# Performance work log

Measured on AMD Instinct MI355X. Metric: run time of the kernel, lower is better.

## Reference

```python
import jax, jax.numpy as jnp
import numpy as np

B, N, BS, H, DH, L, FF, V, R = 1, 4096, 64, 12, 64, 4, 3072, 30522, 3
D = H * DH
M = N // BS
NEG = -10000.0


def layernorm(x, g, b, eps=1e-5):
    mu = x.mean(-1, keepdims=True)
    var = ((x - mu) ** 2).mean(-1, keepdims=True)
    return (x - mu) * jax.lax.rsqrt(var + eps) * g + b


def bigbird_attention(q, k, v, band_mask, from_mask, to_mask, blocked_mask, rand_attn):
    # q,k,v: [b,h,n,d]; band_mask [b,1,m-4,BS,3BS]; to_mask [b,1,1,n]; from_mask [b,1,n,1]
    b, h, n, d = q.shape
    m = n // BS
    r = rand_attn.shape[-1]
    sc = 1.0 / jnp.sqrt(jnp.float32(d))
    qb = q.reshape(b, h, m, BS, d)
    kb = k.reshape(b, h, m, BS, d)
    vb = v.reshape(b, h, m, BS, d)
    hid = jnp.arange(h)[:, None, None]
    gk = kb[:, hid, rand_attn].reshape(b, h, m - 2, r * BS, d)  # gathered random keys
    gv = vb[:, hid, rand_attn].reshape(b, h, m - 2, r * BS, d)
    rand_to = blocked_mask[:, rand_attn].reshape(b, h, m - 2, r * BS)
    rand_mask = jnp.einsum('blq,bhlk->bhlqk', blocked_mask[:, 1:-1], rand_to)  # [b,h,m-2,BS,rBS]

    # first block: dense over all keys (global)
    s = jnp.einsum('bhqd,bhkd->bhqk', qb[:, :, 0], k) * sc + (1.0 - to_mask) * NEG
    c_first = jnp.einsum('bhqk,bhkd->bhqd', jax.nn.softmax(s, axis=-1), v)

    # second block: blocks 0,1,2, last, + random row 0
    k2 = jnp.concatenate([kb[:, :, 0], kb[:, :, 1], kb[:, :, 2], kb[:, :, -1], gk[:, :, 0]], axis=2)
    v2 = jnp.concatenate([vb[:, :, 0], vb[:, :, 1], vb[:, :, 2], vb[:, :, -1], gv[:, :, 0]], axis=2)
    s = jnp.einsum('bhqd,bhkd->bhqk', qb[:, :, 1], k2) * sc
    seq_pad = jnp.concatenate([to_mask[..., :3 * BS], to_mask[..., -BS:],
                               jnp.ones((b, 1, 1, r * BS), s.dtype)], axis=3)
    rnd_pad = jnp.concatenate([jnp.ones((b, h, BS, 4 * BS), s.dtype), rand_mask[:, :, 0]], axis=3)
    s = s + (1.0 - jnp.minimum(seq_pad, rnd_pad)) * NEG
    c_second = jnp.einsum('bhqk,bhkd->bhqd', jax.nn.softmax(s, axis=-1), v2)

    # middle blocks: first-global + 3-block band + random + last-global
    mq = qb[:, :, 2:-2]  # [b,h,m-4,BS,d]
    exp_k = jnp.concatenate([kb[:, :, 1:-3], kb[:, :, 2:-2], kb[:, :, 3:-1]], axis=3)
    exp_v = jnp.concatenate([vb[:, :, 1:-3], vb[:, :, 2:-2], vb[:, :, 3:-1]], axis=3)
    inner = jnp.einsum('bhlqd,bhlkd->bhlqk', mq, exp_k) * sc + (1.0 - band_mask) * NEG
    randp = jnp.einsum('bhlqd,bhlkd->bhlqk', mq, gk[:, :, 1:-1]) * sc + (1.0 - rand_mask[:, :, 1:-1]) * NEG
    firstp = jnp.einsum('bhlqd,bhkd->bhlqk', mq, kb[:, :, 0]) * sc + (1.0 - to_mask[:, :, None, :, :BS]) * NEG
    lastp = jnp.einsum('bhlqd,bhkd->bhlqk', mq, kb[:, :, -1]) * sc + (1.0 - to_mask[:, :, None, :, -BS:]) * NEG
    w = jax.nn.softmax(jnp.concatenate([firstp, inner, randp, lastp], axis=-1), axis=-1)
    c_mid = jnp.einsum('bhlqk,bhlkd->bhlqd', w[..., BS:4 * BS], exp_v)
    c_mid = c_mid + jnp.einsum('bhlqk,bhlkd->bhlqd', w[..., 4 * BS:4 * BS + r * BS], gv[:, :, 1:-1])
    c_mid = c_mid + jnp.einsum('bhlqk,bhkd->bhlqd', w[..., :BS], vb[:, :, 0])
    c_mid = c_mid + jnp.einsum('bhlqk,bhkd->bhlqd', w[..., -BS:], vb[:, :, -1])

    # second-to-last block: block 0, last 3 blocks, + random row -1
    k3 = jnp.concatenate([kb[:, :, 0], kb[:, :, -3], kb[:, :, -2], kb[:, :, -1], gk[:, :, -1]], axis=2)
    v3 = jnp.concatenate([vb[:, :, 0], vb[:, :, -3], vb[:, :, -2], vb[:, :, -1], gv[:, :, -1]], axis=2)
    s = jnp.einsum('bhqd,bhkd->bhqk', qb[:, :, -2], k3) * sc
    seq_pad = jnp.concatenate([to_mask[..., :BS], to_mask[..., -3 * BS:],
                               jnp.ones((b, 1, 1, r * BS), s.dtype)], axis=3)
    rnd_pad = jnp.concatenate([jnp.ones((b, h, BS, 4 * BS), s.dtype), rand_mask[:, :, -1]], axis=3)
    s = s + (1.0 - jnp.minimum(seq_pad, rnd_pad)) * NEG
    c_sl = jnp.einsum('bhqk,bhkd->bhqd', jax.nn.softmax(s, axis=-1), v3)

    # last block: dense over all keys (global)
    s = jnp.einsum('bhqd,bhkd->bhqk', qb[:, :, -1], k) * sc + (1.0 - to_mask) * NEG
    c_last = jnp.einsum('bhqk,bhkd->bhqd', jax.nn.softmax(s, axis=-1), v)

    ctx = jnp.concatenate([c_first[:, :, None], c_second[:, :, None], c_mid,
                           c_sl[:, :, None], c_last[:, :, None]], axis=2)
    ctx = ctx.reshape(b, h, n, d) * from_mask
    return ctx.transpose(0, 2, 1, 3).reshape(b, n, h * d)


def forward(input_ids, mask, rand_attn, emb_word, emb_pos, emb_ln_g, emb_ln_b,
            Wq, bq, Wk, bk, Wv, bv, Wo, bo, ln1_g, ln1_b, W1, b1, W2, b2, ln2_g, ln2_b):
    b, n = input_ids.shape
    m = n // BS
    x = emb_word[input_ids] + emb_pos[None, :n]
    x = layernorm(x, emb_ln_g, emb_ln_b)
    blocked_mask = mask.reshape(b, m, BS)
    exp_to = jnp.concatenate([blocked_mask[:, 1:-3], blocked_mask[:, 2:-2], blocked_mask[:, 3:-1]], axis=2)
    band_mask = jnp.einsum('blq,blk->blqk', blocked_mask[:, 2:-2], exp_to)[:, None]
    from_mask = mask.reshape(b, 1, n, 1)
    to_mask = mask.reshape(b, 1, 1, n)
    for i in range(L):
        q = (x @ Wq[i] + bq[i]).reshape(b, n, H, DH).transpose(0, 2, 1, 3)
        k = (x @ Wk[i] + bk[i]).reshape(b, n, H, DH).transpose(0, 2, 1, 3)
        v = (x @ Wv[i] + bv[i]).reshape(b, n, H, DH).transpose(0, 2, 1, 3)
        a = bigbird_attention(q, k, v, band_mask, from_mask, to_mask, blocked_mask, rand_attn)
        a = a @ Wo[i] + bo[i]
        x = layernorm(x + a, ln1_g[i], ln1_b[i])  # dropout is identity in eval
        f = jax.nn.gelu(x @ W1[i] + b1[i], approximate=False) @ W2[i] + b2[i]
        x = layernorm(x + f, ln2_g[i], ln2_b[i])
    return x


def setup_inputs() -> dict:
    key = jax.random.key(0)
    ks = jax.random.split(key, 12)
    s = 0.02
    nrm = lambda k, shape: jax.random.normal(k, shape, jnp.float32) * s
    rng = np.random.default_rng(0)
    rand_attn = jnp.asarray(rng.integers(1, M - 1, size=(H, M - 2, R)), jnp.int32)
    return {
        'input_ids': jax.random.randint(ks[0], (B, N), 0, V),
        'mask': jnp.ones((B, N), jnp.float32),
        'rand_attn': rand_attn,
        'emb_word': nrm(ks[1], (V, D)),
        'emb_pos': nrm(ks[2], (N, D)),
        'emb_ln_g': jnp.ones((D,), jnp.float32), 'emb_ln_b': jnp.zeros((D,), jnp.float32),
        'Wq': nrm(ks[3], (L, D, D)), 'bq': jnp.zeros((L, D), jnp.float32),
        'Wk': nrm(ks[4], (L, D, D)), 'bk': jnp.zeros((L, D), jnp.float32),
        'Wv': nrm(ks[5], (L, D, D)), 'bv': jnp.zeros((L, D), jnp.float32),
        'Wo': nrm(ks[6], (L, D, D)), 'bo': jnp.zeros((L, D), jnp.float32),
        'ln1_g': jnp.ones((L, D), jnp.float32), 'ln1_b': jnp.zeros((L, D), jnp.float32),
        'W1': nrm(ks[7], (L, D, FF)), 'b1': jnp.zeros((L, FF), jnp.float32),
        'W2': nrm(ks[8], (L, FF, D)), 'b2': jnp.zeros((L, D), jnp.float32),
        'ln2_g': jnp.ones((L, D), jnp.float32), 'ln2_b': jnp.zeros((L, D), jnp.float32),
    }


def reference(input_ids, mask, rand_attn, emb_word, emb_pos, emb_ln_g, emb_ln_b,
              Wq, bq, Wk, bk, Wv, bv, Wo, bo, ln1_g, ln1_b, W1, b1, W2, b2, ln2_g, ln2_b):
    return forward(input_ids, mask, rand_attn, emb_word, emb_pos, emb_ln_g, emb_ln_b,
                   Wq, bq, Wk, bk, Wv, bv, Wo, bo, ln1_g, ln1_b, W1, b1, W2, b2, ln2_g, ln2_b)
```

## Files before the change

### kernel.cpp

```cpp
#include <hip/hip_runtime.h>
#include <hip/hip_bf16.h>
#include <math.h>

#define NTOK   4096
#define DMODEL 768
#define NHEAD  12
#define DHEAD  64
#define NLAYER 4
#define DFF    3072
#define NBLK   64
#define NEGC   -10000.0f

using frag8 = __attribute__((ext_vector_type(8))) short;
using f32x4 = __attribute__((ext_vector_type(4))) float;

typedef __attribute__((address_space(3))) void       lds_void;
typedef const __attribute__((address_space(1))) void gbl_void;

__device__ __forceinline__ void gload_lds16(const void* g, void* l) {
  __builtin_amdgcn_global_load_lds((gbl_void*)g, (lds_void*)l, 16, 0, 0);
}

__device__ __forceinline__ float block_sum256(float v) {
  __shared__ float tmp[4];
  #pragma unroll
  for (int o = 32; o > 0; o >>= 1) v += __shfl_down(v, o, 64);
  __syncthreads();
  if ((threadIdx.x & 63) == 0) tmp[threadIdx.x >> 6] = v;
  __syncthreads();
  return tmp[0] + tmp[1] + tmp[2] + tmp[3];
}

__global__ __launch_bounds__(256) void embed_ln_kernel(
    const int* __restrict__ ids, const float* __restrict__ emb_word,
    const float* __restrict__ emb_pos, const float* __restrict__ g,
    const float* __restrict__ b, float* __restrict__ x,
    __hip_bfloat16* __restrict__ xb)
{
  const int n = blockIdx.x;
  const int tid = threadIdx.x;
  const int id = ids[n];
  float v[3];
  #pragma unroll
  for (int j = 0; j < 3; ++j) {
    int d = tid + j * 256;
    v[j] = emb_word[(size_t)id * DMODEL + d] + emb_pos[(size_t)n * DMODEL + d];
  }
  float mu = block_sum256(v[0] + v[1] + v[2]) * (1.0f / DMODEL);
  float var = 0.f;
  #pragma unroll
  for (int j = 0; j < 3; ++j) { float t = v[j] - mu; var += t * t; }
  var = block_sum256(var) * (1.0f / DMODEL);
  float rs = rsqrtf(var + 1e-5f);
  #pragma unroll
  for (int j = 0; j < 3; ++j) {
    int d = tid + j * 256;
    float o = (v[j] - mu) * rs * g[d] + b[d];
    x[(size_t)n * DMODEL + d] = o;
    xb[(size_t)n * DMODEL + d] = (__hip_bfloat16)o;
  }
}

__global__ __launch_bounds__(256) void add_ln_red_kernel(
    const float* __restrict__ xin, const float* __restrict__ P, size_t ps,
    int nparts, const float* __restrict__ bias2,
    const float* __restrict__ g, const float* __restrict__ b,
    float* __restrict__ dst, __hip_bfloat16* __restrict__ dstb)
{
  const int n = blockIdx.x;
  const int tid = threadIdx.x;
  float v[3];
  #pragma unroll
  for (int j = 0; j < 3; ++j) {
    int d = tid + j * 256;
    float s = xin[(size_t)n * DMODEL + d] + bias2[d];
    for (int z = 0; z < nparts; ++z)
      s += P[(size_t)z * ps + (size_t)n * DMODEL + d];
    v[j] = s;
  }
  float mu = block_sum256(v[0] + v[1] + v[2]) * (1.0f / DMODEL);
  float var = 0.f;
  #pragma unroll
  for (int j = 0; j < 3; ++j) { float t = v[j] - mu; var += t * t; }
  var = block_sum256(var) * (1.0f / DMODEL);
  float rs = rsqrtf(var + 1e-5f);
  #pragma unroll
  for (int j = 0; j < 3; ++j) {
    int d = tid + j * 256;
    float ov = (v[j] - mu) * rs * g[d] + b[d];
    dst[(size_t)n * DMODEL + d] = ov;
    dstb[(size_t)n * DMODEL + d] = (__hip_bfloat16)ov;
  }
}

__global__ __launch_bounds__(256) void transpose_w_kernel(
    const float* __restrict__ W, __hip_bfloat16* __restrict__ WT, int K, int N)
{
  __shared__ float tile[32][33];
  const int n0 = blockIdx.x * 32;
  const int k0 = blockIdx.y * 32;
  const int c = threadIdx.x & 31;
  const int r0 = threadIdx.x >> 5;
  #pragma unroll
  for (int i = 0; i < 4; ++i) {
    int r = r0 + i * 8;
    tile[r][c] = W[(size_t)(k0 + r) * N + n0 + c];
  }
  __syncthreads();
  #pragma unroll
  for (int i = 0; i < 4; ++i) {
    int r = r0 + i * 8;
    WT[(size_t)(n0 + r) * K + k0 + c] = (__hip_bfloat16)tile[c][r];
  }
}

__global__ __launch_bounds__(256) void pack_bias_kernel(
    const float* __restrict__ bq, const float* __restrict__ bk,
    const float* __restrict__ bv, float* __restrict__ dst)
{
  int t = blockIdx.x * 256 + threadIdx.x;
  if (t < 3 * DMODEL)
    dst[t] = (t < DMODEL) ? bq[t] : (t < 2 * DMODEL ? bk[t - DMODEL] : bv[t - 2 * DMODEL]);
}

__global__ __launch_bounds__(256) void gemm_bf16_kernel(
    const __hip_bfloat16* __restrict__ A, int lda,
    const __hip_bfloat16* __restrict__ BT, int ldb,
    const float* __restrict__ bias,
    float* __restrict__ Cf, size_t cfStride,
    __hip_bfloat16* __restrict__ Cb,
    int Kpart, int ldC, int do_gelu)
{
  __shared__ __hip_bfloat16 Als[2][64 * 32];
  __shared__ __hip_bfloat16 Bls[2][128 * 32];
  const int tid = threadIdx.x;

  const int gx = gridDim.x;
  const int nwg = gx * gridDim.y;
  const int orig = blockIdx.y * gx + blockIdx.x;
  const int q = nwg >> 3, r = nwg & 7;
  const int xcd = orig & 7, loc = orig >> 3;
  const int wg = (xcd < r ? xcd * (q + 1) : r * (q + 1) + (xcd - r) * q) + loc;
  const int bm = (wg % gx) * 64;
  const int bn = (wg / gx) * 128;
  const int z  = blockIdx.z;
  const int koff = z * Kpart;

  const int wave = tid >> 6, lane = tid & 63;
  const int wm = (wave >> 1) * 32, wn = (wave & 1) * 64;
  const int lm = lane & 15, quad = lane >> 4;

  const int rA = wave * 16 + (lane >> 2);
  const int kc = (lane & 3) * 8;

  const __hip_bfloat16* Ar  = A  + (size_t)(bm + rA) * lda + koff + kc;
  const __hip_bfloat16* Br0 = BT + (size_t)(bn + rA) * ldb + koff + kc;
  const __hip_bfloat16* Br1 = BT + (size_t)(bn + 64 + rA) * ldb + koff + kc;

  f32x4 acc[2][4];
  #pragma unroll
  for (int i = 0; i < 2; ++i)
    #pragma unroll
    for (int j = 0; j < 4; ++j)
      acc[i][j] = (f32x4){0.f, 0.f, 0.f, 0.f};

  gload_lds16(Ar,  &Als[0][rA * 32 + kc]);
  gload_lds16(Br0, &Bls[0][rA * 32 + kc]);
  gload_lds16(Br1, &Bls[0][(64 + rA) * 32 + kc]);

  int p = 0;
  for (int k0 = 0; k0 < Kpart; k0 += 32, p ^= 1) {
    __syncthreads();
    const int kn = k0 + 32;
    if (kn < Kpart) {
      gload_lds16(Ar + kn,  &Als[p ^ 1][rA * 32 + kc]);
      gload_lds16(Br0 + kn, &Bls[p ^ 1][rA * 32 + kc]);
      gload_lds16(Br1 + kn, &Bls[p ^ 1][(64 + rA) * 32 + kc]);
    }
    frag8 afr[2], bfr[4];
    #pragma unroll
    for (int mt = 0; mt < 2; ++mt)
      afr[mt] = *(const frag8*)(&Als[p][(wm + mt * 16 + lm) * 32 + quad * 8]);
    #pragma unroll
    for (int nt = 0; nt < 4; ++nt)
      bfr[nt] = *(const frag8*)(&Bls[p][(wn + nt * 16 + lm) * 32 + quad * 8]);
    #pragma unroll
    for (int mt = 0; mt < 2; ++mt)
      #pragma unroll
      for (int nt = 0; nt < 4; ++nt)
        acc[mt][nt] = __builtin_amdgcn_mfma_f32_16x16x32_bf16(
            afr[mt], bfr[nt], acc[mt][nt], 0, 0, 0);
  }

  float* Cfz = Cf ? Cf + (size_t)z * cfStride : nullptr;
  #pragma unroll
  for (int mt = 0; mt < 2; ++mt)
    #pragma unroll
    for (int nt = 0; nt < 4; ++nt)
      #pragma unroll
      for (int rr = 0; rr < 4; ++rr) {
        int row = bm + wm + mt * 16 + quad * 4 + rr;
        int col = bn + wn + nt * 16 + lm;
        float v = acc[mt][nt][rr];
        if (bias) v += bias[col];
        if (do_gelu) v = 0.5f * v * (1.f + erff(v * 0.70710678118654752f));
        if (Cfz) Cfz[(size_t)row * ldC + col] = v;
        if (Cb) Cb[(size_t)row * ldC + col] = (__hip_bfloat16)v;
      }
}

__global__ __launch_bounds__(256) void attn_kernel(
    const __hip_bfloat16* __restrict__ qkvb, const float* __restrict__ mask,
    const int* __restrict__ rand_attn, __hip_bfloat16* __restrict__ outp,
    float* __restrict__ Mpart, float* __restrict__ Lpart, float* __restrict__ Opart)
{
  const int h = blockIdx.x;
  const int item = blockIdx.y;
  const int tid = threadIdx.x;

  int qi, chunk;
  if (item < 8)       { qi = 0;        chunk = item; }
  else if (item < 70) { qi = item - 7; chunk = -1; }
  else                { qi = 63;       chunk = item - 70; }

  __shared__ __hip_bfloat16 Qs[64 * 72];
  __shared__ __hip_bfloat16 Ks[64 * 72];
  __shared__ __hip_bfloat16 VTs[64 * 72];
  __shared__ __hip_bfloat16 Ps[64 * 72];
  __shared__ int slist[8];
  __shared__ int snb;

  const __hip_bfloat16* qg = qkvb;
  const __hip_bfloat16* kg = qkvb + DMODEL;
  const __hip_bfloat16* vg = qkvb + 2 * DMODEL;
  const int ldq = 3 * DMODEL;

  const int wave = tid >> 6, lane = tid & 63;
  const int wm = wave * 16;
  const int lm = lane & 15, quad = lane >> 4;

  {
    int r = tid >> 2, c0 = (tid & 3) * 16;
    const __hip_bfloat16* qp = qg + (size_t)(qi * 64 + r) * ldq + h * 64 + c0;
    uint4 a = *(const uint4*)qp;
    uint4 b = *(const uint4*)(qp + 8);
    *(uint4*)(Qs + r * 72 + c0) = a;
    *(uint4*)(Qs + r * 72 + c0 + 8) = b;
  }
  if (tid == 0) {
    if (chunk >= 0) {
      for (int j = 0; j < 8; ++j) slist[j] = chunk * 8 + j;
      snb = 8;
    } else {
      const int* ra = rand_attn + ((size_t)h * 62 + (qi - 1)) * 3;
      if (qi == 1)       { slist[0] = 0; slist[1] = 1;  slist[2] = 2;  slist[3] = 63; }
      else if (qi == 62) { slist[0] = 0; slist[1] = 61; slist[2] = 62; slist[3] = 63; }
      else               { slist[0] = 0; slist[1] = qi - 1; slist[2] = qi; slist[3] = qi + 1; }
      slist[4] = ra[0]; slist[5] = ra[1]; slist[6] = ra[2];
      int nb = 7;
      if (qi >= 2 && qi <= 61) { slist[7] = 63; nb = 8; }
      snb = nb;
    }
  }
  __syncthreads();
  const int nb = snb;

  frag8 aq0 = *(const frag8*)(Qs + (wm + lm) * 72 + quad * 8);
  frag8 aq1 = *(const frag8*)(Qs + (wm + lm) * 72 + 32 + quad * 8);

  float mold[4], lsum[4];
  #pragma unroll
  for (int r = 0; r < 4; ++r) { mold[r] = -1e30f; lsum[r] = 0.f; }
  f32x4 oacc[4];
  #pragma unroll
  for (int t = 0; t < 4; ++t) oacc[t] = (f32x4){0.f, 0.f, 0.f, 0.f};

  const int sr = tid >> 2, sc0 = (tid & 3) * 16;

  for (int bi = 0; bi < nb; ++bi) {
    const int kb = slist[bi];
    const __hip_bfloat16* kp = kg + (size_t)(kb * 64 + sr) * ldq + h * 64 + sc0;
    const __hip_bfloat16* vp = vg + (size_t)(kb * 64 + sr) * ldq + h * 64 + sc0;
    uint4 kv0 = *(const uint4*)kp;
    uint4 kv1 = *(const uint4*)(kp + 8);
    uint4 vv0 = *(const uint4*)vp;
    uint4 vv1 = *(const uint4*)(vp + 8);
    float msk[4];
    #pragma unroll
    for (int t = 0; t < 4; ++t) msk[t] = mask[kb * 64 + t * 16 + lm];

    __syncthreads();
    *(uint4*)(Ks + sr * 72 + sc0) = kv0;
    *(uint4*)(Ks + sr * 72 + sc0 + 8) = kv1;
    {
      union { uint4 u[2]; __hip_bfloat16 h16[16]; } vu;
      vu.u[0] = vv0; vu.u[1] = vv1;
      #pragma unroll
      for (int j = 0; j < 16; ++j)
        VTs[(sc0 + j) * 72 + sr] = vu.h16[j];
    }
    __syncthreads();

    f32x4 sacc[4];
    #pragma unroll
    for (int t = 0; t < 4; ++t) sacc[t] = (f32x4){0.f, 0.f, 0.f, 0.f};
    #pragma unroll
    for (int t = 0; t < 4; ++t) {
      frag8 bk0 = *(const frag8*)(Ks + (t * 16 + lm) * 72 + quad * 8);
      frag8 bk1 = *(const frag8*)(Ks + (t * 16 + lm) * 72 + 32 + quad * 8);
      sacc[t] = __builtin_amdgcn_mfma_f32_16x16x32_bf16(aq0, bk0, sacc[t], 0, 0, 0);
      sacc[t] = __builtin_amdgcn_mfma_f32_16x16x32_bf16(aq1, bk1, sacc[t], 0, 0, 0);
    }

    float xs[4][4];
    #pragma unroll
    for (int t = 0; t < 4; ++t)
      #pragma unroll
      for (int r = 0; r < 4; ++r)
        xs[t][r] = sacc[t][r] * 0.125f + (1.f - msk[t]) * NEGC;

    float al[4], psum[4];
    #pragma unroll
    for (int r = 0; r < 4; ++r) {
      float rm = fmaxf(fmaxf(xs[0][r], xs[1][r]), fmaxf(xs[2][r], xs[3][r]));
      rm = fmaxf(rm, __shfl_xor(rm, 1, 64));
      rm = fmaxf(rm, __shfl_xor(rm, 2, 64));
      rm = fmaxf(rm, __shfl_xor(rm, 4, 64));
      rm = fmaxf(rm, __shfl_xor(rm, 8, 64));
      float mnew = fmaxf(mold[r], rm);
      al[r] = __expf(mold[r] - mnew);
      float s = 0.f;
      #pragma unroll
      for (int t = 0; t < 4; ++t) {
        float p = __expf(xs[t][r] - mnew);
        xs[t][r] = p;
        s += p;
      }
      s += __shfl_xor(s, 1, 64);
      s += __shfl_xor(s, 2, 64);
      s += __shfl_xor(s, 4, 64);
      s += __shfl_xor(s, 8, 64);
      psum[r] = s;
      mold[r] = mnew;
    }
    #pragma unroll
    for (int r = 0; r < 4; ++r) lsum[r] = lsum[r] * al[r] + psum[r];
    #pragma unroll
    for (int t = 0; t < 4; ++t)
      #pragma unroll
      for (int r = 0; r < 4; ++r)
        oacc[t][r] *= al[r];

    #pragma unroll
    for (int t = 0; t < 4; ++t)
      #pragma unroll
      for (int r = 0; r < 4; ++r)
        Ps[(wm + quad * 4 + r) * 72 + t * 16 + lm] = (__hip_bfloat16)xs[t][r];

    frag8 ap0 = *(const frag8*)(Ps + (wm + lm) * 72 + quad * 8);
    frag8 ap1 = *(const frag8*)(Ps + (wm + lm) * 72 + 32 + quad * 8);
    #pragma unroll
    for (int t = 0; t < 4; ++t) {
      frag8 bv0 = *(const frag8*)(VTs + (t * 16 + lm) * 72 + quad * 8);
      frag8 bv1 = *(const frag8*)(VTs + (t * 16 + lm) * 72 + 32 + quad * 8);
      oacc[t] = __builtin_amdgcn_mfma_f32_16x16x32_bf16(ap0, bv0, oacc[t], 0, 0, 0);
      oacc[t] = __builtin_amdgcn_mfma_f32_16x16x32_bf16(ap1, bv1, oacc[t], 0, 0, 0);
    }
  }

  if (chunk < 0) {
    #pragma unroll
    for (int r = 0; r < 4; ++r) {
      int row = qi * 64 + wm + quad * 4 + r;
      float sc2 = mask[row] / lsum[r];
      #pragma unroll
      for (int t = 0; t < 4; ++t)
        outp[(size_t)row * DMODEL + h * 64 + t * 16 + lm] =
            (__hip_bfloat16)(oacc[t][r] * sc2);
    }
  } else {
    const int idx = (h * 2 + (qi == 63 ? 1 : 0)) * 8 + chunk;
    #pragma unroll
    for (int r = 0; r < 4; ++r) {
      int row = wm + quad * 4 + r;
      #pragma unroll
      for (int t = 0; t < 4; ++t)
        Opart[(size_t)idx * 4096 + row * 64 + t * 16 + lm] = oacc[t][r];
      if (lm == 0) {
        Mpart[idx * 64 + row] = mold[r];
        Lpart[idx * 64 + row] = lsum[r];
      }
    }
  }
}

__global__ __launch_bounds__(256) void attn_merge_kernel(
    const float* __restrict__ Mpart, const float* __restrict__ Lpart,
    const float* __restrict__ Opart, const float* __restrict__ mask,
    __hip_bfloat16* __restrict__ outp)
{
  const int h = blockIdx.x, side = blockIdx.y;
  const int qi = side ? 63 : 0;
  const int tid = threadIdx.x;
  const int r = tid >> 2;
  const int d0 = (tid & 3) * 16;
  const int base = (h * 2 + side) * 8;

  float mv[8], m = -1e30f;
  #pragma unroll
  for (int c = 0; c < 8; ++c) { mv[c] = Mpart[(base + c) * 64 + r]; m = fmaxf(m, mv[c]); }
  float sc[8], l = 0.f;
  #pragma unroll
  for (int c = 0; c < 8; ++c) {
    sc[c] = __expf(mv[c] - m);
    l += Lpart[(base + c) * 64 + r] * sc[c];
  }
  float o[16];
  #pragma unroll
  for (int d = 0; d < 16; ++d) o[d] = 0.f;
  #pragma unroll
  for (int c = 0; c < 8; ++c) {
    const float* Op = Opart + (size_t)(base + c) * 4096 + r * 64 + d0;
    #pragma unroll
    for (int d4 = 0; d4 < 4; ++d4) {
      float4 v4 = *(const float4*)(Op + d4 * 4);
      o[d4 * 4 + 0] += v4.x * sc[c];
      o[d4 * 4 + 1] += v4.y * sc[c];
      o[d4 * 4 + 2] += v4.z * sc[c];
      o[d4 * 4 + 3] += v4.w * sc[c];
    }
  }
  const int row = qi * 64 + r;
  float inv = mask[row] / l;
  #pragma unroll
  for (int d = 0; d < 16; ++d)
    outp[(size_t)row * DMODEL + h * 64 + d0 + d] = (__hip_bfloat16)(o[d] * inv);
}

extern "C" void kernel_launch(void* const* d_in, const int* in_sizes, int n_in,
                              void* d_out, int out_size, void* d_ws, size_t ws_size,
                              hipStream_t stream)
{
  const int*   ids      = (const int*)  d_in[0];
  const float* mask     = (const float*)d_in[1];
  const int*   rand_att = (const int*)  d_in[2];
  const float* emb_word = (const float*)d_in[3];
  const float* emb_pos  = (const float*)d_in[4];
  const float* eg       = (const float*)d_in[5];
  const float* eb       = (const float*)d_in[6];
  const float* Wq = (const float*)d_in[7];
  const float* bq = (const float*)d_in[8];
  const float* Wk = (const float*)d_in[9];
  const float* bk = (const float*)d_in[10];
  const float* Wv = (const float*)d_in[11];
  const float* bv = (const float*)d_in[12];
  const float* Wo = (const float*)d_in[13];
  const float* bo = (const float*)d_in[14];
  const float* ln1g = (const float*)d_in[15];
  const float* ln1b = (const float*)d_in[16];
  const float* W1 = (const float*)d_in[17];
  const float* bf1 = (const float*)d_in[18];
  const float* W2 = (const float*)d_in[19];
  const float* bf2 = (const float*)d_in[20];
  const float* ln2g = (const float*)d_in[21];
  const float* ln2b = (const float*)d_in[22];

  const size_t ND = (size_t)NTOK * DMODEL;
  float* x   = (float*)d_ws;
  __hip_bfloat16* xb = (__hip_bfloat16*)(x + ND);
  float* P   = (float*)(xb + ND);
  __hip_bfloat16* qkvb = (__hip_bfloat16*)(P + 3 * ND);
  __hip_bfloat16* fb_b = qkvb + 3 * ND;
  __hip_bfloat16* ab_b = fb_b + (size_t)NTOK * DFF;
  __hip_bfloat16* wqkvT = ab_b + ND;
  __hip_bfloat16* woT  = wqkvT + (size_t)3 * DMODEL * DMODEL;
  __hip_bfloat16* w1T  = woT  + (size_t)DMODEL * DMODEL;
  __hip_bfloat16* w2T  = w1T  + (size_t)DFF * DMODEL;
  float* biasf = (float*)(w2T + (size_t)DMODEL * DFF);
  float* Mpart = biasf + 3 * DMODEL;
  float* Lpart = Mpart + NHEAD * 2 * 8 * 64;
  float* Opart = Lpart + NHEAD * 2 * 8 * 64;

  embed_ln_kernel<<<NTOK, 256, 0, stream>>>(ids, emb_word, emb_pos, eg, eb, x, xb);

  for (int l = 0; l < NLAYER; ++l) {
    const float* Wq_l = Wq + (size_t)l * DMODEL * DMODEL;
    const float* Wk_l = Wk + (size_t)l * DMODEL * DMODEL;
    const float* Wv_l = Wv + (size_t)l * DMODEL * DMODEL;
    const float* Wo_l = Wo + (size_t)l * DMODEL * DMODEL;
    const float* W1_l = W1 + (size_t)l * DMODEL * DFF;
    const float* W2_l = W2 + (size_t)l * DFF * DMODEL;

    dim3 g32(DMODEL / 32, DMODEL / 32);
    transpose_w_kernel<<<g32, 256, 0, stream>>>(Wq_l, wqkvT, DMODEL, DMODEL);
    transpose_w_kernel<<<g32, 256, 0, stream>>>(Wk_l, wqkvT + (size_t)DMODEL * DMODEL, DMODEL, DMODEL);
    transpose_w_kernel<<<g32, 256, 0, stream>>>(Wv_l, wqkvT + (size_t)2 * DMODEL * DMODEL, DMODEL, DMODEL);
    transpose_w_kernel<<<g32, 256, 0, stream>>>(Wo_l, woT, DMODEL, DMODEL);
    transpose_w_kernel<<<dim3(DFF / 32, DMODEL / 32), 256, 0, stream>>>(W1_l, w1T, DMODEL, DFF);
    transpose_w_kernel<<<dim3(DMODEL / 32, DFF / 32), 256, 0, stream>>>(W2_l, w2T, DFF, DMODEL);
    pack_bias_kernel<<<9, 256, 0, stream>>>(bq + (size_t)l * DMODEL, bk + (size_t)l * DMODEL,
                                            bv + (size_t)l * DMODEL, biasf);

    gemm_bf16_kernel<<<dim3(NTOK / 64, 3 * DMODEL / 128, 1), 256, 0, stream>>>(
        xb, DMODEL, wqkvT, DMODEL, biasf, nullptr, 0, qkvb, DMODEL, 3 * DMODEL, 0);

    attn_kernel<<<dim3(NHEAD, 78), 256, 0, stream>>>(qkvb, mask, rand_att, ab_b,
                                                     Mpart, Lpart, Opart);
    attn_merge_kernel<<<dim3(NHEAD, 2), 256, 0, stream>>>(Mpart, Lpart, Opart, mask, ab_b);

    gemm_bf16_kernel<<<dim3(NTOK / 64, DMODEL / 128, 2), 256, 0, stream>>>(
        ab_b, DMODEL, woT, DMODEL, nullptr, P, ND, nullptr, DMODEL / 2, DMODEL, 0);
    add_ln_red_kernel<<<NTOK, 256, 0, stream>>>(x, P, ND, 2, bo + (size_t)l * DMODEL,
                                                ln1g + (size_t)l * DMODEL,
                                                ln1b + (size_t)l * DMODEL, x, xb);

    gemm_bf16_kernel<<<dim3(NTOK / 64, DFF / 128, 1), 256, 0, stream>>>(
        xb, DMODEL, w1T, DMODEL, bf1 + (size_t)l * DFF, nullptr, 0, fb_b, DMODEL, DFF, 1);

    gemm_bf16_kernel<<<dim3(NTOK / 64, DMODEL / 128, 3), 256, 0, stream>>>(
        fb_b, DFF, w2T, DFF, nullptr, P, ND, nullptr, DFF / 3, DMODEL, 0);
    add_ln_red_kernel<<<NTOK, 256, 0, stream>>>(x, P, ND, 3, bf2 + (size_t)l * DMODEL,
                                                ln2g + (size_t)l * DMODEL,
                                                ln2b + (size_t)l * DMODEL,
                                                (l == NLAYER - 1) ? (float*)d_out : x, xb);
  }
}
```

Before: 1.172 ms.

## Add 256x256 swizzled-LDS GEMM for QKV/FF1 and fuse weight prep launches

Adds a 512-thread GEMM kernel with 256x256 output tiles, 64-wide K steps, XOR-swizzled LDS staging and an interleaved load/MFMA schedule using barriers and setprio. It is used for the QKV and FF1 projections, raising data reuse per block and cutting LDS bank conflicts. The six per-layer transpose launches and the bias-pack launch are merged into one prep kernel to reduce launch overhead. The large tiles give only 144–192 workgroups on a 256-CU device, so part of the GPU may sit idle, and the 128KB LDS allocation limits occupancy to one block per CU.

```diff
diff --git a/kernel.cpp b/kernel.cpp
--- a/kernel.cpp
+++ b/kernel.cpp
@@ -93,34 +93,54 @@
   }
 }
 
-__global__ __launch_bounds__(256) void transpose_w_kernel(
-    const float* __restrict__ W, __hip_bfloat16* __restrict__ WT, int K, int N)
-{
+__global__ __launch_bounds__(256) void prep_weights_kernel(
+    const float* __restrict__ Wq, const float* __restrict__ Wk,
+    const float* __restrict__ Wv, const float* __restrict__ Wo,
+    const float* __restrict__ W1, const float* __restrict__ W2,
+    const float* __restrict__ bq, const float* __restrict__ bk,
+    const float* __restrict__ bv,
+    __hip_bfloat16* __restrict__ wqkvT, __hip_bfloat16* __restrict__ woT,
+    __hip_bfloat16* __restrict__ w1T, __hip_bfloat16* __restrict__ w2T,
+    float* __restrict__ biasf)
+{
+  const int id = blockIdx.x;
+  if (id >= 6912) {
+    int t = (id - 6912) * 256 + threadIdx.x;
+    if (t < 3 * DMODEL)
+      biasf[t] = (t < DMODEL) ? bq[t] : (t < 2 * DMODEL ? bk[t - DMODEL] : bv[t - 2 * DMODEL]);
+    return;
+  }
+  const float* src;
+  __hip_bfloat16* dst;
+  int K, N, local;
+  if (id < 2304) {
+    int m = id / 576; local = id % 576;
+    src = (m == 0) ? Wq : (m == 1) ? Wk : (m == 2) ? Wv : Wo;
+    dst = (m < 3) ? wqkvT + (size_t)m * DMODEL * DMODEL : woT;
+    K = DMODEL; N = DMODEL;
+  } else if (id < 4608) {
+    local = id - 2304; src = W1; dst = w1T; K = DMODEL; N = DFF;
+  } else {
+    local = id - 4608; src = W2; dst = w2T; K = DFF; N = DMODEL;
+  }
+  const int ntiles = N / 32;
+  const int n0 = (local % ntiles) * 32;
+  const int k0 = (local / ntiles) * 32;
+
   __shared__ float tile[32][33];
-  const int n0 = blockIdx.x * 32;
-  const int k0 = blockIdx.y * 32;
   const int c = threadIdx.x & 31;
   const int r0 = threadIdx.x >> 5;
   #pragma unroll
   for (int i = 0; i < 4; ++i) {
     int r = r0 + i * 8;
-    tile[r][c] = W[(size_t)(k0 + r) * N + n0 + c];
+    tile[r][c] = src[(size_t)(k0 + r) * N + n0 + c];
   }
   __syncthreads();
   #pragma unroll
   for (int i = 0; i < 4; ++i) {
     int r = r0 + i * 8;
-    WT[(size_t)(n0 + r) * K + k0 + c] = (__hip_bfloat16)tile[c][r];
-  }
-}
-
-__global__ __launch_bounds__(256) void pack_bias_kernel(
-    const float* __restrict__ bq, const float* __restrict__ bk,
-    const float* __restrict__ bv, float* __restrict__ dst)
-{
-  int t = blockIdx.x * 256 + threadIdx.x;
-  if (t < 3 * DMODEL)
-    dst[t] = (t < DMODEL) ? bq[t] : (t < 2 * DMODEL ? bk[t - DMODEL] : bv[t - 2 * DMODEL]);
+    dst[(size_t)(n0 + r) * K + k0 + c] = (__hip_bfloat16)tile[c][r];
+  }
 }
 
 __global__ __launch_bounds__(256) void gemm_bf16_kernel(
@@ -179,8 +199,8 @@
     }
     frag8 afr[2], bfr[4];
     #pragma unroll
-    for (int mt = 0; mt < 2; ++mt)
-      afr[mt] = *(const frag8*)(&Als[p][(wm + mt * 16 + lm) * 32 + quad * 8]);
+    for (int t = 0; t < 2; ++t)
+      afr[t] = *(const frag8*)(&Als[p][(wm + t * 16 + lm) * 32 + quad * 8]);
     #pragma unroll
     for (int nt = 0; nt < 4; ++nt)
       bfr[nt] = *(const frag8*)(&Bls[p][(wn + nt * 16 + lm) * 32 + quad * 8]);
@@ -206,6 +226,147 @@
         if (do_gelu) v = 0.5f * v * (1.f + erff(v * 0.70710678118654752f));
         if (Cfz) Cfz[(size_t)row * ldC + col] = v;
         if (Cb) Cb[(size_t)row * ldC + col] = (__hip_bfloat16)v;
+      }
+}
+
+__global__ __launch_bounds__(512, 2) void gemm256_kernel(
+    const __hip_bfloat16* __restrict__ A, int lda,
+    const __hip_bfloat16* __restrict__ BT,
+    const float* __restrict__ bias,
+    __hip_bfloat16* __restrict__ Cb, int ldC,
+    int K, int do_gelu)
+{
+  __shared__ uint4 smem4[131072 / 16];
+  char* lds = (char*)smem4;
+  const int tid = threadIdx.x;
+  const int bm = blockIdx.x * 256;
+  const int bn = blockIdx.y * 256;
+  const int wave = tid >> 6, lane = tid & 63;
+  const int wm = wave >> 2;
+  const int wn = wave & 3;
+  const int lm = lane & 15, quad = lane >> 4;
+
+  const int srow = tid >> 3;
+  const int schx = ((tid & 7) ^ (srow & 7)) * 16;
+  const int ldst0 = tid * 16;
+  const int ldst1 = 8192 + tid * 16;
+  const char* Abytes = (const char*)A;
+  const char* Bbytes = (const char*)BT;
+  const size_t ldab = (size_t)lda * 2;
+
+  const int co0 = ((0 + quad) ^ (lm & 7)) * 16;
+  const int co1 = ((4 + quad) ^ (lm & 7)) * 16;
+
+  f32x4 acc[8][4];
+  #pragma unroll
+  for (int i = 0; i < 8; ++i)
+    #pragma unroll
+    for (int j = 0; j < 4; ++j)
+      acc[i][j] = (f32x4){0.f, 0.f, 0.f, 0.f};
+
+#define STAGE(BASE, ROW0, LOFF, KB) do {                                      \
+    const char* _s = (BASE) + (size_t)((ROW0) + srow) * ldab + (KB) + schx;   \
+    gload_lds16(_s, lds + (LOFF) + ldst0);                                    \
+    gload_lds16(_s + 64 * ldab, lds + (LOFF) + ldst1);                        \
+  } while (0)
+
+  STAGE(Abytes, bm,        0,             (size_t)0);
+  STAGE(Abytes, bm + 128,  16384,         (size_t)0);
+  STAGE(Bbytes, bn,        65536,         (size_t)0);
+  STAGE(Bbytes, bn + 128,  65536 + 16384, (size_t)0);
+
+  frag8 a[4][2], b[2][2];
+
+#define RD_A(MTB) do {                                                        \
+    _Pragma("unroll")                                                         \
+    for (int mt = 0; mt < 4; ++mt) {                                          \
+      const char* ap = Ab + (size_t)((wm * 128 + ((MTB) + mt) * 16 + lm) * 128); \
+      a[mt][0] = *(const frag8*)(ap + co0);                                   \
+      a[mt][1] = *(const frag8*)(ap + co1);                                   \
+    } } while (0)
+#define RD_B(NTB) do {                                                        \
+    _Pragma("unroll")                                                         \
+    for (int nt = 0; nt < 2; ++nt) {                                          \
+      const char* bp = Bb + (size_t)((wn * 64 + ((NTB) + nt) * 16 + lm) * 128); \
+      b[nt][0] = *(const frag8*)(bp + co0);                                   \
+      b[nt][1] = *(const frag8*)(bp + co1);                                   \
+    } } while (0)
+#define MMQ(MTB, NTB) do {                                                    \
+    _Pragma("unroll")                                                         \
+    for (int mt = 0; mt < 4; ++mt)                                            \
+      _Pragma("unroll")                                                       \
+      for (int nt = 0; nt < 2; ++nt) {                                        \
+        acc[(MTB) + mt][(NTB) + nt] = __builtin_amdgcn_mfma_f32_16x16x32_bf16( \
+            a[mt][0], b[nt][0], acc[(MTB) + mt][(NTB) + nt], 0, 0, 0);        \
+        acc[(MTB) + mt][(NTB) + nt] = __builtin_amdgcn_mfma_f32_16x16x32_bf16( \
+            a[mt][1], b[nt][1], acc[(MTB) + mt][(NTB) + nt], 0, 0, 0);        \
+      } } while (0)
+
+  const int NT = K >> 6;
+  for (int t = 0; t < NT; ++t) {
+    const int p = t & 1;
+    const char* Ab = lds + p * 32768;
+    const char* Bb = lds + 65536 + p * 32768;
+    const int qb_ = (p ^ 1) * 32768;
+    const size_t kb = (size_t)(t + 1) * 128;
+    const bool more = (t + 1 < NT);
+
+    if (more) {
+      STAGE(Abytes, bm, qb_, kb);
+      asm volatile("s_waitcnt vmcnt(2)" ::: "memory");
+    } else {
+      asm volatile("s_waitcnt vmcnt(0)" ::: "memory");
+    }
+    __builtin_amdgcn_sched_barrier(0);
+    __builtin_amdgcn_s_barrier();
+    __builtin_amdgcn_sched_barrier(0);
+    RD_A(0); RD_B(0);
+    __builtin_amdgcn_s_setprio(1);
+    MMQ(0, 0);
+    __builtin_amdgcn_s_setprio(0);
+    __builtin_amdgcn_s_barrier();
+
+    RD_B(2);
+    if (more) STAGE(Abytes, bm + 128, qb_ + 16384, kb);
+    __builtin_amdgcn_s_barrier();
+    __builtin_amdgcn_s_setprio(1);
+    MMQ(0, 2);
+    __builtin_amdgcn_s_setprio(0);
+    __builtin_amdgcn_s_barrier();
+
+    RD_A(4);
+    if (more) STAGE(Bbytes, bn, 65536 + qb_, kb);
+    __builtin_amdgcn_s_barrier();
+    __builtin_amdgcn_s_setprio(1);
+    MMQ(4, 2);
+    __builtin_amdgcn_s_setprio(0);
+    __builtin_amdgcn_s_barrier();
+
+    RD_B(0);
+    if (more) STAGE(Bbytes, bn + 128, 65536 + qb_ + 16384, kb);
+    __builtin_amdgcn_s_barrier();
+    __builtin_amdgcn_s_setprio(1);
+    MMQ(4, 0);
+    __builtin_amdgcn_s_setprio(0);
+    __builtin_amdgcn_s_barrier();
+  }
+
+#undef STAGE
+#undef RD_A
+#undef RD_B
+#undef MMQ
+
+  #pragma unroll
+  for (int mt = 0; mt < 8; ++mt)
+    #pragma unroll
+    for (int nt = 0; nt < 4; ++nt)
+      #pragma unroll
+      for (int rr = 0; rr < 4; ++rr) {
+        int row = bm + wm * 128 + mt * 16 + quad * 4 + rr;
+        int col = bn + wn * 64 + nt * 16 + lm;
+        float v = acc[mt][nt][rr] + bias[col];
+        if (do_gelu) v = 0.5f * v * (1.f + erff(v * 0.70710678118654752f));
+        Cb[(size_t)row * ldC + col] = (__hip_bfloat16)v;
       }
 }
 
@@ -491,18 +652,13 @@
     const float* W1_l = W1 + (size_t)l * DMODEL * DFF;
     const float* W2_l = W2 + (size_t)l * DFF * DMODEL;
 
-    dim3 g32(DMODEL / 32, DMODEL / 32);
-    transpose_w_kernel<<<g32, 256, 0, stream>>>(Wq_l, wqkvT, DMODEL, DMODEL);
-    transpose_w_kernel<<<g32, 256, 0, stream>>>(Wk_l, wqkvT + (size_t)DMODEL * DMODEL, DMODEL, DMODEL);
-    transpose_w_kernel<<<g32, 256, 0, stream>>>(Wv_l, wqkvT + (size_t)2 * DMODEL * DMODEL, DMODEL, DMODEL);
-    transpose_w_kernel<<<g32, 256, 0, stream>>>(Wo_l, woT, DMODEL, DMODEL);
-    transpose_w_kernel<<<dim3(DFF / 32, DMODEL / 32), 256, 0, stream>>>(W1_l, w1T, DMODEL, DFF);
-    transpose_w_kernel<<<dim3(DMODEL / 32, DFF / 32), 256, 0, stream>>>(W2_l, w2T, DFF, DMODEL);
-    pack_bias_kernel<<<9, 256, 0, stream>>>(bq + (size_t)l * DMODEL, bk + (size_t)l * DMODEL,
-                                            bv + (size_t)l * DMODEL, biasf);
-
-    gemm_bf16_kernel<<<dim3(NTOK / 64, 3 * DMODEL / 128, 1), 256, 0, stream>>>(
-        xb, DMODEL, wqkvT, DMODEL, biasf, nullptr, 0, qkvb, DMODEL, 3 * DMODEL, 0);
+    prep_weights_kernel<<<6921, 256, 0, stream>>>(
+        Wq_l, Wk_l, Wv_l, Wo_l, W1_l, W2_l,
+        bq + (size_t)l * DMODEL, bk + (size_t)l * DMODEL, bv + (size_t)l * DMODEL,
+        wqkvT, woT, w1T, w2T, biasf);
+
+    gemm256_kernel<<<dim3(NTOK / 256, 3 * DMODEL / 256), 512, 0, stream>>>(
+        xb, DMODEL, wqkvT, biasf, qkvb, 3 * DMODEL, DMODEL, 0);
 
     attn_kernel<<<dim3(NHEAD, 78), 256, 0, stream>>>(qkvb, mask, rand_att, ab_b,
                                                      Mpart, Lpart, Opart);
@@ -514,8 +670,8 @@
                                                 ln1g + (size_t)l * DMODEL,
                                                 ln1b + (size_t)l * DMODEL, x, xb);
 
-    gemm_bf16_kernel<<<dim3(NTOK / 64, DFF / 128, 1), 256, 0, stream>>>(
-        xb, DMODEL, w1T, DMODEL, bf1 + (size_t)l * DFF, nullptr, 0, fb_b, DMODEL, DFF, 1);
+    gemm256_kernel<<<dim3(NTOK / 256, DFF / 256), 512, 0, stream>>>(
+        xb, DMODEL, w1T, bf1 + (size_t)l * DFF, fb_b, DFF, DMODEL, 1);
 
     gemm_bf16_kernel<<<dim3(NTOK / 64, DMODEL / 128, 3), 256, 0, stream>>>(
         fb_b, DFF, w2T, DFF, nullptr, P, ND, nullptr, DFF / 3, DMODEL, 0);
```

After: 1.084 ms. -7.5%, faster.
